# Kernel tuning notes

Measured on AMD Instinct MI355X. Metric: run time of the kernel, lower is better.

The kernel has to match this reference:

```python
import jax, jax.numpy as jnp
import numpy as np

C = 256; NH = 8; HD = C // NH; NL = 4; NP = 4; DFF = 1024
B = 8; NQ = 900
SHAPES = ((100, 100), (50, 50), (25, 25), (13, 13))
LEN = sum(h * w for h, w in SHAPES)


def setup_inputs() -> dict:
    key = jax.random.key(0)
    ks = jax.random.split(key, 16)
    s = 0.02
    d = {}
    d['tgt'] = jax.random.normal(ks[0], (B, NQ, C), jnp.float32)
    d['query_pos'] = jax.random.normal(ks[1], (B, NQ, C), jnp.float32)
    d['reference_points'] = jax.random.uniform(ks[2], (B, NQ, NL, 2), jnp.float32)
    d['src'] = jax.random.normal(ks[3], (B, LEN, C), jnp.float32)
    d['spatial_shapes'] = np.array(SHAPES, dtype=np.int32)
    # self-attn (nn.MultiheadAttention) params, stored [in,out]
    d['sa_in_w'] = jax.random.normal(ks[4], (C, 3 * C), jnp.float32) * s
    d['sa_in_b'] = jnp.zeros((3 * C,), jnp.float32)
    d['sa_out_w'] = jax.random.normal(ks[5], (C, C), jnp.float32) * s
    d['sa_out_b'] = jnp.zeros((C,), jnp.float32)
    d['ln2_g'] = jnp.ones((C,), jnp.float32); d['ln2_b'] = jnp.zeros((C,), jnp.float32)
    # MSDeformAttn params
    d['off_w'] = jax.random.normal(ks[6], (C, NH * NL * NP * 2), jnp.float32) * s
    d['off_b'] = jax.random.normal(ks[7], (NH * NL * NP * 2,), jnp.float32) * 0.5
    d['attw_w'] = jax.random.normal(ks[8], (C, NH * NL * NP), jnp.float32) * s
    d['attw_b'] = jnp.zeros((NH * NL * NP,), jnp.float32)
    d['val_w'] = jax.random.normal(ks[9], (C, C), jnp.float32) * s
    d['val_b'] = jnp.zeros((C,), jnp.float32)
    d['proj_w'] = jax.random.normal(ks[10], (C, C), jnp.float32) * s
    d['proj_b'] = jnp.zeros((C,), jnp.float32)
    d['ln1_g'] = jnp.ones((C,), jnp.float32); d['ln1_b'] = jnp.zeros((C,), jnp.float32)
    # FFN
    d['lin1_w'] = jax.random.normal(ks[11], (C, DFF), jnp.float32) * s
    d['lin1_b'] = jnp.zeros((DFF,), jnp.float32)
    d['lin2_w'] = jax.random.normal(ks[12], (DFF, C), jnp.float32) * s
    d['lin2_b'] = jnp.zeros((C,), jnp.float32)
    d['ln3_g'] = jnp.ones((C,), jnp.float32); d['ln3_b'] = jnp.zeros((C,), jnp.float32)
    return d


def _ln(x, g, b):
    m = jnp.mean(x, -1, keepdims=True)
    v = jnp.mean((x - m) ** 2, -1, keepdims=True)
    return (x - m) * jax.lax.rsqrt(v + 1e-5) * g + b


def _bilinear(v, loc, H, W):
    # v: [B,NH,H*W,HD]; loc: [B,NQ,NH,NP,2] normalized to [0,1]
    # matches F.grid_sample(align_corners=False, padding_mode='zeros')
    b = v.shape[0]; nq = loc.shape[1]
    x = loc[..., 0] * W - 0.5
    y = loc[..., 1] * H - 0.5
    x0 = jnp.floor(x); y0 = jnp.floor(y)
    dx = x - x0; dy = y - y0
    x0i = x0.astype(jnp.int32); y0i = y0.astype(jnp.int32)

    def gat(ix, iy):
        valid = ((ix >= 0) & (ix < W) & (iy >= 0) & (iy < H)).astype(v.dtype)
        idx = jnp.clip(iy, 0, H - 1) * W + jnp.clip(ix, 0, W - 1)  # [B,NQ,NH,NP]
        idx_t = jnp.transpose(idx, (0, 2, 1, 3)).reshape(b, NH, nq * NP)
        g = jnp.take_along_axis(v, idx_t[..., None], axis=2).reshape(b, NH, nq, NP, HD)
        return g * jnp.transpose(valid, (0, 2, 1, 3))[..., None]

    wt = lambda a: jnp.transpose(a, (0, 2, 1, 3))[..., None]
    return (gat(x0i, y0i) * wt((1 - dx) * (1 - dy))
            + gat(x0i + 1, y0i) * wt(dx * (1 - dy))
            + gat(x0i, y0i + 1) * wt((1 - dx) * dy)
            + gat(x0i + 1, y0i + 1) * wt(dx * dy))


def _msda(q, ref, src, shapes, val_w, val_b, off_w, off_b, attw_w, attw_b, proj_w, proj_b):
    b, nq, _ = q.shape
    value = jnp.transpose((src @ val_w + val_b).reshape(b, -1, NH, HD), (0, 2, 1, 3))  # [B,NH,Len,HD]
    off = (q @ off_w + off_b).reshape(b, nq, NH, NL, NP, 2)
    aw = jax.nn.softmax((q @ attw_w + attw_b).reshape(b, nq, NH, NL * NP), -1)
    aw = aw.reshape(b, nq, NH, NL, NP)
    acc = jnp.zeros((b, NH, nq, HD), q.dtype)
    start = 0
    for l, (H_, W_) in enumerate(shapes):
        norm = jnp.array([W_, H_], q.dtype)
        loc = ref[:, :, None, l, None, :] + off[:, :, :, l] / norm  # [B,NQ,NH,NP,2]
        smp = _bilinear(value[:, :, start:start + H_ * W_], loc, H_, W_)  # [B,NH,NQ,NP,HD]
        acc = acc + jnp.sum(smp * jnp.transpose(aw[:, :, :, l], (0, 2, 1, 3))[..., None], axis=3)
        start += H_ * W_
    out = jnp.transpose(acc, (0, 2, 1, 3)).reshape(b, nq, C)
    return out @ proj_w + proj_b


def _self_attn(x, pos, in_w, in_b, out_w, out_b):
    b, nq, _ = x.shape
    qk = x + pos
    q = (qk @ in_w[:, :C] + in_b[:C]).reshape(b, nq, NH, HD)
    k = (qk @ in_w[:, C:2 * C] + in_b[C:2 * C]).reshape(b, nq, NH, HD)
    v = (x @ in_w[:, 2 * C:] + in_b[2 * C:]).reshape(b, nq, NH, HD)
    att = jax.nn.softmax(jnp.einsum('bqhd,bkhd->bhqk', q, k) * (1.0 / float(np.sqrt(HD))), -1)
    o = jnp.einsum('bhqk,bkhd->bqhd', att, v).reshape(b, nq, C)
    return o @ out_w + out_b


def _forward(tgt, query_pos, reference_points, src, shapes,
             sa_in_w, sa_in_b, sa_out_w, sa_out_b, ln2_g, ln2_b,
             off_w, off_b, attw_w, attw_b, val_w, val_b, proj_w, proj_b, ln1_g, ln1_b,
             lin1_w, lin1_b, lin2_w, lin2_b, ln3_g, ln3_b):
    t2 = _self_attn(tgt, query_pos, sa_in_w, sa_in_b, sa_out_w, sa_out_b)
    t = _ln(tgt + t2, ln2_g, ln2_b)
    t2 = _msda(t + query_pos, reference_points, src, shapes,
               val_w, val_b, off_w, off_b, attw_w, attw_b, proj_w, proj_b)
    t = _ln(t + t2, ln1_g, ln1_b)
    h = jax.nn.relu(t @ lin1_w + lin1_b) @ lin2_w + lin2_b
    return _ln(t + h, ln3_g, ln3_b)


def reference(tgt, query_pos, reference_points, src, spatial_shapes,
              sa_in_w, sa_in_b, sa_out_w, sa_out_b, ln2_g, ln2_b,
              off_w, off_b, attw_w, attw_b, val_w, val_b, proj_w, proj_b, ln1_g, ln1_b,
              lin1_w, lin1_b, lin2_w, lin2_b, ln3_g, ln3_b):
    shapes = [(int(h), int(w)) for h, w in np.asarray(spatial_shapes)]
    return _forward(tgt, query_pos, reference_points, src, shapes,
                    sa_in_w, sa_in_b, sa_out_w, sa_out_b, ln2_g, ln2_b,
                    off_w, off_b, attw_w, attw_b, val_w, val_b, proj_w, proj_b, ln1_g, ln1_b,
                    lin1_w, lin1_b, lin2_w, lin2_b, ln3_g, ln3_b)
```

## Files before the change

### kernel.cpp

```cpp
#include <hip/hip_runtime.h>
#include <hip/hip_bf16.h>
#include <type_traits>

#define C_DIM 256
#define NHEAD 8
#define HDIM 32
#define NLVL 4
#define NPT 4
#define DFF_DIM 1024
#define BB 8
#define NQ_DIM 900
#define LEN_DIM 13294
#define ROWS (BB * NQ_DIM)
#define VROWS (BB * LEN_DIM)
#define VT_LD 928

typedef __attribute__((ext_vector_type(8))) short short8v;
typedef __attribute__((ext_vector_type(8))) unsigned short ushort8v;
typedef __attribute__((ext_vector_type(4))) float float4v;
typedef __attribute__((ext_vector_type(4))) unsigned short ushort4v;

__device__ __forceinline__ float bf2f(unsigned short u) {
  union { unsigned int i; float f; } v; v.i = ((unsigned int)u) << 16; return v.f;
}
__device__ __forceinline__ unsigned short f2bf(float f) {
  __hip_bfloat16 h = __float2bfloat16(f);
  return *reinterpret_cast<unsigned short*>(&h);
}

#define WCONV_BLOCKS 2048
__global__ __launch_bounds__(256) void wprep_kernel(
    const float* __restrict__ w0, const float* __restrict__ w1,
    const float* __restrict__ w2, const float* __restrict__ w3,
    const float* __restrict__ w4, const float* __restrict__ w5,
    const float* __restrict__ w6, const float* __restrict__ w7,
    unsigned short* __restrict__ out,
    const float* __restrict__ tgt, const float* __restrict__ qpos,
    unsigned short* __restrict__ tgtbf, unsigned short* __restrict__ x0bf, int n4) {
  int bid = blockIdx.x;
  if (bid < WCONV_BLOCKS) {
    const int Ks[8] = {256, 256, 256, 256, 256, 256, 256, 1024};
    const int Ns[8] = {768, 256, 256, 128, 256, 256, 1024, 256};
    const int Oo[8] = {0, 196608, 262144, 327680, 360448, 425984, 491520, 753664};
    int w = bid >> 8, bx = bid & 255;
    int K = Ks[w], N = Ns[w];
    int ntx = N >> 5, nty = K >> 5;
    if (bx >= ntx * nty) return;
    int tx = bx % ntx, ty = bx / ntx;
    const float* W = w == 0 ? w0 : w == 1 ? w1 : w == 2 ? w2 : w == 3 ? w3
                   : w == 4 ? w4 : w == 5 ? w5 : w == 6 ? w6 : w7;
    __shared__ float tile[32][33];
    int c = threadIdx.x & 31, rg = threadIdx.x >> 5;
#pragma unroll
    for (int j = 0; j < 4; ++j) {
      int k = ty * 32 + rg * 4 + j;
      tile[rg * 4 + j][c] = W[(size_t)k * N + tx * 32 + c];
    }
    __syncthreads();
    unsigned short* o = out + Oo[w];
#pragma unroll
    for (int j = 0; j < 4; ++j) {
      int n = tx * 32 + rg * 4 + j;
      o[(size_t)n * K + ty * 32 + c] = f2bf(tile[c][rg * 4 + j]);
    }
  } else {
    int i = (bid - WCONV_BLOCKS) * 256 + threadIdx.x;
    if (i < n4) {
      float4 x = reinterpret_cast<const float4*>(tgt)[i];
      float4 y = reinterpret_cast<const float4*>(qpos)[i];
      ushort4v u1, u2;
      u1[0] = f2bf(x.x); u1[1] = f2bf(x.y); u1[2] = f2bf(x.z); u1[3] = f2bf(x.w);
      u2[0] = f2bf(x.x + y.x); u2[1] = f2bf(x.y + y.y);
      u2[2] = f2bf(x.z + y.z); u2[3] = f2bf(x.w + y.w);
      *reinterpret_cast<ushort4v*>(tgtbf + (size_t)i * 4) = u1;
      *reinterpret_cast<ushort4v*>(x0bf + (size_t)i * 4) = u2;
    }
  }
}

template <typename TA, typename TO, int RELU>
__device__ __forceinline__ void gemm_body(
    unsigned short* smem,
    const TA* __restrict__ A, const TA* __restrict__ A2,
    const unsigned short* __restrict__ Wt,
    const float* __restrict__ bias, const float* __restrict__ bias2,
    TO* __restrict__ Cout, TO* __restrict__ Cout2,
    int M, int N, int K, int lda, int ldc, int ldc2, int colSplit,
    int bx, int by) {
  auto Al = reinterpret_cast<unsigned short(*)[128][40]>(smem);
  auto Wl = reinterpret_cast<unsigned short(*)[128][40]>(smem + 10240);
  const int tid = threadIdx.x;
  const int lane = tid & 63, wid = tid >> 6;
  const int g = lane >> 4, ql = lane & 15;
  const int wr = wid >> 1, wc = wid & 1;
  const int row0 = by * 128, col0 = bx * 128;

  const TA* Ause = (A2 != nullptr && col0 >= colSplit) ? A2 : A;

  float4v acc[4][4];
#pragma unroll
  for (int i = 0; i < 4; ++i)
#pragma unroll
    for (int j = 0; j < 4; ++j) acc[i][j] = (float4v){0.f, 0.f, 0.f, 0.f};

  float4 areg_f[4];
  ushort8v areg_b[2];
  ushort8v wreg[2];

  auto loadA = [&](int k0) {
    if constexpr (std::is_same<TA, float>::value) {
#pragma unroll
      for (int j = 0; j < 4; ++j) {
        int c = tid + 256 * j;
        int row = c >> 3, f4 = c & 7;
        int gr = min(row0 + row, M - 1);
        areg_f[j] = *reinterpret_cast<const float4*>(Ause + (size_t)gr * lda + k0 + f4 * 4);
      }
    } else {
#pragma unroll
      for (int j = 0; j < 2; ++j) {
        int c = tid + 256 * j;
        int row = c >> 2, ch = c & 3;
        int gr = min(row0 + row, M - 1);
        areg_b[j] = *reinterpret_cast<const ushort8v*>(
            reinterpret_cast<const unsigned short*>(Ause) + (size_t)gr * lda + k0 + ch * 8);
      }
    }
  };
  auto loadW = [&](int k0) {
#pragma unroll
    for (int j = 0; j < 2; ++j) {
      int c = tid + 256 * j;
      int row = c >> 2, ch = c & 3;
      wreg[j] = *reinterpret_cast<const ushort8v*>(
          Wt + (size_t)(col0 + row) * K + k0 + ch * 8);
    }
  };
  auto storeA = [&](int buf) {
    if constexpr (std::is_same<TA, float>::value) {
#pragma unroll
      for (int j = 0; j < 4; ++j) {
        int c = tid + 256 * j;
        int row = c >> 3, f4 = c & 7;
        ushort4v u;
        u[0] = f2bf(areg_f[j].x); u[1] = f2bf(areg_f[j].y);
        u[2] = f2bf(areg_f[j].z); u[3] = f2bf(areg_f[j].w);
        *reinterpret_cast<ushort4v*>(&Al[buf][row][f4 * 4]) = u;
      }
    } else {
#pragma unroll
      for (int j = 0; j < 2; ++j) {
        int c = tid + 256 * j;
        int row = c >> 2, ch = c & 3;
        *reinterpret_cast<ushort8v*>(&Al[buf][row][ch * 8]) = areg_b[j];
      }
    }
  };
  auto storeW = [&](int buf) {
#pragma unroll
    for (int j = 0; j < 2; ++j) {
      int c = tid + 256 * j;
      int row = c >> 2, ch = c & 3;
      *reinterpret_cast<ushort8v*>(&Wl[buf][row][ch * 8]) = wreg[j];
    }
  };

  const int nt = K >> 5;
  loadA(0); loadW(0);
  storeA(0); storeW(0);

  for (int t = 0; t < nt; ++t) {
    __syncthreads();
    if (t + 1 < nt) { loadA((t + 1) << 5); loadW((t + 1) << 5); }
    const int cur = t & 1;
    short8v af[4], bfr[4];
#pragma unroll
    for (int mi = 0; mi < 4; ++mi)
      af[mi] = *reinterpret_cast<const short8v*>(&Al[cur][wr * 64 + mi * 16 + ql][8 * g]);
#pragma unroll
    for (int ni = 0; ni < 4; ++ni)
      bfr[ni] = *reinterpret_cast<const short8v*>(&Wl[cur][wc * 64 + ni * 16 + ql][8 * g]);
#pragma unroll
    for (int mi = 0; mi < 4; ++mi)
#pragma unroll
      for (int ni = 0; ni < 4; ++ni)
        acc[mi][ni] = __builtin_amdgcn_mfma_f32_16x16x32_bf16(af[mi], bfr[ni], acc[mi][ni], 0, 0, 0);
    if (t + 1 < nt) { storeA(cur ^ 1); storeW(cur ^ 1); }
  }

  const bool sel2 = (Cout2 != nullptr && col0 >= colSplit);
  const float* bsrc = sel2 ? bias2 : bias;
  TO* outp = sel2 ? Cout2 : Cout;
  const int ldco = sel2 ? ldc2 : ldc;
  const int cbase = sel2 ? (col0 - colSplit) : col0;
  float bv[4];
#pragma unroll
  for (int ni = 0; ni < 4; ++ni) bv[ni] = bsrc[cbase + wc * 64 + ni * 16 + ql];
#pragma unroll
  for (int mi = 0; mi < 4; ++mi) {
#pragma unroll
    for (int r = 0; r < 4; ++r) {
      int row = row0 + wr * 64 + mi * 16 + 4 * g + r;
      if (row >= M) continue;
#pragma unroll
      for (int ni = 0; ni < 4; ++ni) {
        int col = cbase + wc * 64 + ni * 16 + ql;
        float v = acc[mi][ni][r] + bv[ni];
        if (RELU) v = fmaxf(v, 0.f);
        if constexpr (std::is_same<TO, float>::value) {
          outp[(size_t)row * ldco + col] = v;
        } else {
          outp[(size_t)row * ldco + col] = __float2bfloat16(v);
        }
      }
    }
  }
}

template <typename TA, typename TO, int RELU>
__global__ __launch_bounds__(256) void mfma_gemm_kernel(
    const TA* __restrict__ A, const TA* __restrict__ A2,
    const unsigned short* __restrict__ Wt,
    const float* __restrict__ bias, const float* __restrict__ bias2,
    TO* __restrict__ Cout, TO* __restrict__ Cout2,
    int M, int N, int K, int lda, int ldc, int ldc2, int colSplit) {
  __shared__ unsigned short smem[20480];
  gemm_body<TA, TO, RELU>(smem, A, A2, Wt, bias, bias2, Cout, Cout2,
                          M, N, K, lda, ldc, ldc2, colSplit,
                          blockIdx.x, blockIdx.y);
}

#define QKV_BLOCKS (6 * 57)
__global__ __launch_bounds__(256) void qkv_value_kernel(
    const unsigned short* __restrict__ x0bf, const unsigned short* __restrict__ tgtbf,
    const unsigned short* __restrict__ sa_inT, const float* __restrict__ sa_in_b,
    __hip_bfloat16* __restrict__ qkbuf, __hip_bfloat16* __restrict__ vbuf,
    const float* __restrict__ src, const unsigned short* __restrict__ valT,
    const float* __restrict__ val_b, __hip_bfloat16* __restrict__ value) {
  __shared__ unsigned short smem[20480];
  int bid = blockIdx.x;
  if (bid < QKV_BLOCKS) {
    gemm_body<unsigned short, __hip_bfloat16, 0>(
        smem, x0bf, tgtbf, sa_inT, sa_in_b, sa_in_b + 512, qkbuf, vbuf,
        ROWS, 768, 256, 256, 512, 256, 512, bid % 6, bid / 6);
  } else {
    int t = bid - QKV_BLOCKS;
    gemm_body<float, __hip_bfloat16, 0>(
        smem, src, nullptr, valT, val_b, nullptr, value, nullptr,
        VROWS, 256, 256, 256, 256, 0, 1 << 30, t & 1, t >> 1);
  }
}

__global__ __launch_bounds__(256) void vtrans_kernel(
    const unsigned short* __restrict__ vbuf, unsigned short* __restrict__ vT) {
  __shared__ unsigned short tile[32][34];
  int b = blockIdx.y;
  int ct = blockIdx.x & 7;
  int rt = blockIdx.x >> 3;
  int rl = threadIdx.x >> 3, c4 = (threadIdx.x & 7) * 4;
  int gr = min(rt * 32 + rl, NQ_DIM - 1);
  ushort4v v = *reinterpret_cast<const ushort4v*>(
      vbuf + ((size_t)(b * NQ_DIM + gr)) * 256 + ct * 32 + c4);
  tile[rl][c4] = v[0]; tile[rl][c4 + 1] = v[1];
  tile[rl][c4 + 2] = v[2]; tile[rl][c4 + 3] = v[3];
  __syncthreads();
  int cl = threadIdx.x >> 3, r4 = (threadIdx.x & 7) * 4;
  ushort4v o;
  o[0] = tile[r4][cl]; o[1] = tile[r4 + 1][cl];
  o[2] = tile[r4 + 2][cl]; o[3] = tile[r4 + 3][cl];
  *reinterpret_cast<ushort4v*>(
      vT + ((size_t)b * 256 + ct * 32 + cl) * VT_LD + rt * 32 + r4) = o;
}

__global__ __launch_bounds__(256) void ln_fused_kernel(const float* __restrict__ x,
                                                       const float* __restrict__ y,
                                                       const float* __restrict__ gg,
                                                       const float* __restrict__ bb,
                                                       float* __restrict__ out,
                                                       unsigned short* __restrict__ out2,
                                                       const float* __restrict__ qadd) {
  int row = blockIdx.x, t = threadIdx.x;
  size_t base = (size_t)row * C_DIM + t;
  float v = x[base] + y[base];
  float s = v, s2 = v * v;
#pragma unroll
  for (int o = 32; o > 0; o >>= 1) {
    s += __shfl_xor(s, o);
    s2 += __shfl_xor(s2, o);
  }
  __shared__ float w1[4], w2[4];
  int wid = t >> 6, lane = t & 63;
  if (lane == 0) { w1[wid] = s; w2[wid] = s2; }
  __syncthreads();
  float S = w1[0] + w1[1] + w1[2] + w1[3];
  float S2 = w2[0] + w2[1] + w2[2] + w2[3];
  float mean = S * (1.f / 256.f);
  float var = S2 * (1.f / 256.f) - mean * mean;
  float rstd = rsqrtf(var + 1e-5f);
  float r = (v - mean) * rstd * gg[t] + bb[t];
  out[base] = r;
  if (out2) {
    float r2 = qadd ? (r + qadd[base]) : r;
    out2[base] = f2bf(r2);
  }
}

__global__ __launch_bounds__(256) void self_attn_mfma_kernel(
    const unsigned short* __restrict__ qk, const unsigned short* __restrict__ vT,
    unsigned short* __restrict__ out) {
  __shared__ unsigned short P_lds[4][16][32];
  const int tid = threadIdx.x;
  const int lane = tid & 63, wid = tid >> 6;
  const int g = lane >> 4, ql = lane & 15;
  const int bh = blockIdx.y;
  const int b = bh >> 3, h = bh & 7;
  const int q0 = blockIdx.x * 64 + wid * 16;
  const float scale = 0.17677669529663687f;

  const unsigned short* qk_b = qk + (size_t)b * NQ_DIM * 512;
  const int qrow = min(q0 + ql, NQ_DIM - 1);
  short8v qf = *reinterpret_cast<const short8v*>(
      qk_b + (size_t)qrow * 512 + h * HDIM + 8 * g);
  const unsigned short* kb = qk_b + 256 + h * HDIM + 8 * g;
  const unsigned short* vtb0 = vT + ((size_t)b * 256 + h * HDIM + ql) * VT_LD;
  const unsigned short* vtb1 = vtb0 + 16 * VT_LD;

  float4v o0 = {0.f, 0.f, 0.f, 0.f}, o1 = {0.f, 0.f, 0.f, 0.f};
  float m = -1e30f, lsum = 0.f;

  const int NT = 29;
  for (int kt = 0; kt < NT; ++kt) {
    const int k_base = kt * 32;
    int kr0 = min(k_base + ql, NQ_DIM - 1);
    int kr1 = min(k_base + 16 + ql, NQ_DIM - 1);
    short8v kf0 = *reinterpret_cast<const short8v*>(kb + (size_t)kr0 * 512);
    short8v kf1 = *reinterpret_cast<const short8v*>(kb + (size_t)kr1 * 512);
    float4v z = {0.f, 0.f, 0.f, 0.f};
    float4v s0 = __builtin_amdgcn_mfma_f32_16x16x32_bf16(kf0, qf, z, 0, 0, 0);
    float4v s1 = __builtin_amdgcn_mfma_f32_16x16x32_bf16(kf1, qf, z, 0, 0, 0);

    float s[8];
#pragma unroll
    for (int r = 0; r < 4; ++r) { s[r] = s0[r] * scale; s[4 + r] = s1[r] * scale; }
    if (kt == NT - 1) {
#pragma unroll
      for (int i = 0; i < 8; ++i) {
        int kk = k_base + 16 * (i >> 2) + 4 * g + (i & 3);
        if (kk >= NQ_DIM) s[i] = -1e30f;
      }
    }
    float tm = s[0];
#pragma unroll
    for (int i = 1; i < 8; ++i) tm = fmaxf(tm, s[i]);
    tm = fmaxf(tm, __shfl_xor(tm, 16));
    tm = fmaxf(tm, __shfl_xor(tm, 32));
    float mnew = fmaxf(m, tm);
    float alpha = __expf(m - mnew);
    float p[8];
    float ts = 0.f;
#pragma unroll
    for (int i = 0; i < 8; ++i) { p[i] = __expf(s[i] - mnew); ts += p[i]; }
    ts += __shfl_xor(ts, 16);
    ts += __shfl_xor(ts, 32);
    lsum = lsum * alpha + ts;
    m = mnew;

    ushort4v pp0, pp1;
#pragma unroll
    for (int r = 0; r < 4; ++r) { pp0[r] = f2bf(p[r]); pp1[r] = f2bf(p[4 + r]); }
    *reinterpret_cast<ushort4v*>(&P_lds[wid][ql][4 * g]) = pp0;
    *reinterpret_cast<ushort4v*>(&P_lds[wid][ql][16 + 4 * g]) = pp1;
    asm volatile("s_waitcnt lgkmcnt(0)" ::: "memory");
    __builtin_amdgcn_sched_barrier(0);

    o0 *= alpha;
    o1 *= alpha;

    short8v pf = *reinterpret_cast<const short8v*>(&P_lds[wid][ql][8 * g]);
    short8v vf0 = *reinterpret_cast<const short8v*>(vtb0 + k_base + 8 * g);
    short8v vf1 = *reinterpret_cast<const short8v*>(vtb1 + k_base + 8 * g);
    o0 = __builtin_amdgcn_mfma_f32_16x16x32_bf16(vf0, pf, o0, 0, 0, 0);
    o1 = __builtin_amdgcn_mfma_f32_16x16x32_bf16(vf1, pf, o1, 0, 0, 0);
  }

  float inv = 1.f / lsum;
  if (q0 + ql < NQ_DIM) {
    unsigned short* op = out + ((size_t)(b * NQ_DIM) + q0 + ql) * C_DIM + h * HDIM;
    ushort4v u0, u1;
#pragma unroll
    for (int r = 0; r < 4; ++r) { u0[r] = f2bf(o0[r] * inv); u1[r] = f2bf(o1[r] * inv); }
    *reinterpret_cast<ushort4v*>(op + 4 * g) = u0;
    *reinterpret_cast<ushort4v*>(op + 16 + 4 * g) = u1;
  }
}

__global__ __launch_bounds__(256) void softmax16_kernel(float* __restrict__ aw, int total) {
  int t = blockIdx.x * 256 + threadIdx.x;
  if (t >= total) return;
  float* p = aw + (size_t)t * 16;
  float vals[16];
  float m = -1e30f;
#pragma unroll
  for (int i = 0; i < 16; ++i) { vals[i] = p[i]; m = fmaxf(m, vals[i]); }
  float s = 0.f;
#pragma unroll
  for (int i = 0; i < 16; ++i) { vals[i] = __expf(vals[i] - m); s += vals[i]; }
  float inv = 1.f / s;
#pragma unroll
  for (int i = 0; i < 16; ++i) p[i] = vals[i] * inv;
}

__global__ __launch_bounds__(256) void msda_sample_kernel(
    const unsigned short* __restrict__ value,
    const float* __restrict__ off,
    const float* __restrict__ aw,
    const float* __restrict__ refp,
    const int* __restrict__ shapes,
    unsigned short* __restrict__ out) {
  int g = blockIdx.x * 64 + (threadIdx.x >> 2);
  int d8 = threadIdx.x & 3;
  int h = g & 7;
  int row = g >> 3;
  int b = row / NQ_DIM;
  float acc[8] = {};
  int start = 0;
  const float* offr = off + (size_t)row * 256 + h * 32;
  const float* awr  = aw + (size_t)row * 128 + h * 16;
  const float* rpr  = refp + (size_t)row * NLVL * 2;
#pragma unroll
  for (int l = 0; l < NLVL; ++l) {
    int Hl = shapes[2 * l], Wl = shapes[2 * l + 1];
    float fx = rpr[2 * l + 0] * (float)Wl - 0.5f;
    float fy = rpr[2 * l + 1] * (float)Hl - 0.5f;
    const unsigned short* vbase =
        value + ((size_t)(b * LEN_DIM + start)) * C_DIM + h * HDIM + d8 * 8;
#pragma unroll
    for (int p = 0; p < NPT; ++p) {
      float x = fx + offr[l * 8 + p * 2];
      float y = fy + offr[l * 8 + p * 2 + 1];
      float a = awr[l * 4 + p];
      float x0f = floorf(x), y0f = floorf(y);
      float dx = x - x0f, dy = y - y0f;
      int x0 = (int)x0f, y0 = (int)y0f;
      int x1 = x0 + 1, y1 = y0 + 1;
      float wx1 = dx, wx0 = 1.f - dx;
      float wy1 = dy * a, wy0 = (1.f - dy) * a;
      bool vx0 = ((unsigned)x0 < (unsigned)Wl);
      bool vx1 = ((unsigned)x1 < (unsigned)Wl);
      bool vy0 = ((unsigned)y0 < (unsigned)Hl);
      bool vy1 = ((unsigned)y1 < (unsigned)Hl);
      float w00 = (vx0 && vy0) ? wx0 * wy0 : 0.f;
      float w10 = (vx1 && vy0) ? wx1 * wy0 : 0.f;
      float w01 = (vx0 && vy1) ? wx0 * wy1 : 0.f;
      float w11 = (vx1 && vy1) ? wx1 * wy1 : 0.f;
      int x0c = min(max(x0, 0), Wl - 1), x1c = min(max(x1, 0), Wl - 1);
      int y0c = min(max(y0, 0), Hl - 1), y1c = min(max(y1, 0), Hl - 1);
      int r0 = y0c * Wl, r1 = y1c * Wl;
      ushort8v g00 = *reinterpret_cast<const ushort8v*>(vbase + ((r0 + x0c) << 8));
      ushort8v g10 = *reinterpret_cast<const ushort8v*>(vbase + ((r0 + x1c) << 8));
      ushort8v g01 = *reinterpret_cast<const ushort8v*>(vbase + ((r1 + x0c) << 8));
      ushort8v g11 = *reinterpret_cast<const ushort8v*>(vbase + ((r1 + x1c) << 8));
#pragma unroll
      for (int j = 0; j < 8; ++j)
        acc[j] += w00 * bf2f(g00[j]) + w10 * bf2f(g10[j]) +
                  w01 * bf2f(g01[j]) + w11 * bf2f(g11[j]);
    }
    start += Hl * Wl;
  }
  ushort8v o;
#pragma unroll
  for (int j = 0; j < 8; ++j) o[j] = f2bf(acc[j]);
  *reinterpret_cast<ushort8v*>(out + (size_t)row * C_DIM + h * HDIM + d8 * 8) = o;
}

extern "C" void kernel_launch(void* const* d_in, const int* in_sizes, int n_in,
                              void* d_out, int out_size, void* d_ws, size_t ws_size,
                              hipStream_t stream) {
  const float* tgt      = (const float*)d_in[0];
  const float* qpos     = (const float*)d_in[1];
  const float* refp     = (const float*)d_in[2];
  const float* src      = (const float*)d_in[3];
  const int*   shapes   = (const int*)d_in[4];
  const float* sa_in_w  = (const float*)d_in[5];
  const float* sa_in_b  = (const float*)d_in[6];
  const float* sa_out_w = (const float*)d_in[7];
  const float* sa_out_b = (const float*)d_in[8];
  const float* ln2_g    = (const float*)d_in[9];
  const float* ln2_b    = (const float*)d_in[10];
  const float* off_w    = (const float*)d_in[11];
  const float* off_b    = (const float*)d_in[12];
  const float* attw_w   = (const float*)d_in[13];
  const float* attw_b   = (const float*)d_in[14];
  const float* val_w    = (const float*)d_in[15];
  const float* val_b    = (const float*)d_in[16];
  const float* proj_w   = (const float*)d_in[17];
  const float* proj_b   = (const float*)d_in[18];
  const float* ln1_g    = (const float*)d_in[19];
  const float* ln1_b    = (const float*)d_in[20];
  const float* lin1_w   = (const float*)d_in[21];
  const float* lin1_b   = (const float*)d_in[22];
  const float* lin2_w   = (const float*)d_in[23];
  const float* lin2_b   = (const float*)d_in[24];
  const float* ln3_g    = (const float*)d_in[25];
  const float* ln3_b    = (const float*)d_in[26];

  char* ws = (char*)d_ws;
  size_t off_b_ws = 0;
  auto alloc = [&](size_t bytes) {
    char* p = ws + off_b_ws;
    off_b_ws += (bytes + 255) & ~(size_t)255;
    return p;
  };
  unsigned short* wT     = (unsigned short*)alloc((size_t)1015808 * 2);
  unsigned short* value  = (unsigned short*)alloc((size_t)VROWS * C_DIM * 2);
  unsigned short* qkbuf  = (unsigned short*)alloc((size_t)ROWS * 512 * 2);
  unsigned short* vbuf   = (unsigned short*)alloc((size_t)ROWS * 256 * 2);
  unsigned short* vTbuf  = (unsigned short*)alloc((size_t)BB * 256 * VT_LD * 2);
  unsigned short* tgtbf  = (unsigned short*)alloc((size_t)ROWS * C_DIM * 2);
  unsigned short* X0bf   = (unsigned short*)alloc((size_t)ROWS * C_DIM * 2);
  unsigned short* attnbf = (unsigned short*)alloc((size_t)ROWS * C_DIM * 2);
  unsigned short* X3bf   = (unsigned short*)alloc((size_t)ROWS * C_DIM * 2);
  unsigned short* sampbf = (unsigned short*)alloc((size_t)ROWS * C_DIM * 2);
  unsigned short* X6bf   = (unsigned short*)alloc((size_t)ROWS * C_DIM * 2);
  unsigned short* hidbf  = (unsigned short*)alloc((size_t)ROWS * DFF_DIM * 2);
  float* X1 = (float*)alloc((size_t)ROWS * C_DIM * 4);
  float* X2 = (float*)alloc((size_t)ROWS * C_DIM * 4);
  float* X4 = (float*)alloc((size_t)ROWS * C_DIM * 4);
  float* X5 = (float*)alloc((size_t)ROWS * 128 * 4);
  float* X6 = (float*)alloc((size_t)ROWS * C_DIM * 4);
  if (off_b_ws > ws_size) return;

  unsigned short* sa_inT = wT + 0;
  unsigned short* sa_outT = wT + 196608;
  unsigned short* offT   = wT + 262144;
  unsigned short* valT   = wT + 360448;
  unsigned short* projT  = wT + 425984;
  unsigned short* lin1T  = wT + 491520;
  unsigned short* lin2T  = wT + 753664;

  dim3 blk(256);
  const int MB7200 = (ROWS + 127) / 128;
  const int MBV = (VROWS + 127) / 128;
  int n4 = ROWS * C_DIM / 4;
  int prepBlocks = (n4 + 255) / 256;

  wprep_kernel<<<WCONV_BLOCKS + prepBlocks, blk, 0, stream>>>(
      sa_in_w, sa_out_w, off_w, attw_w, val_w, proj_w, lin1_w, lin2_w, wT,
      tgt, qpos, tgtbf, X0bf, n4);

  qkv_value_kernel<<<QKV_BLOCKS + 2 * MBV, blk, 0, stream>>>(
      X0bf, tgtbf, sa_inT, sa_in_b, (__hip_bfloat16*)qkbuf, (__hip_bfloat16*)vbuf,
      src, valT, val_b, (__hip_bfloat16*)value);

  vtrans_kernel<<<dim3(8 * 29, BB), blk, 0, stream>>>(vbuf, vTbuf);

  self_attn_mfma_kernel<<<dim3(15, 64), blk, 0, stream>>>(qkbuf, vTbuf, attnbf);
  mfma_gemm_kernel<unsigned short, float, 0><<<dim3(2, MB7200), blk, 0, stream>>>(
      attnbf, nullptr, sa_outT, sa_out_b, nullptr,
      X1, nullptr, ROWS, 256, 256, 256, 256, 0, 1 << 30);
  ln_fused_kernel<<<ROWS, blk, 0, stream>>>(tgt, X1, ln2_g, ln2_b, X2, X3bf, qpos);

  mfma_gemm_kernel<unsigned short, float, 0><<<dim3(3, MB7200), blk, 0, stream>>>(
      X3bf, nullptr, offT, off_b, attw_b,
      X4, X5, ROWS, 384, 256, 256, 256, 128, 256);
  softmax16_kernel<<<(ROWS * NHEAD + 255) / 256, blk, 0, stream>>>(X5, ROWS * NHEAD);
  msda_sample_kernel<<<ROWS * NHEAD / 64, blk, 0, stream>>>(
      value, X4, X5, refp, shapes, sampbf);
  mfma_gemm_kernel<unsigned short, float, 0><<<dim3(2, MB7200), blk, 0, stream>>>(
      sampbf, nullptr, projT, proj_b, nullptr,
      X1, nullptr, ROWS, 256, 256, 256, 256, 0, 1 << 30);
  ln_fused_kernel<<<ROWS, blk, 0, stream>>>(X2, X1, ln1_g, ln1_b, X6, X6bf, nullptr);

  mfma_gemm_kernel<unsigned short, __hip_bfloat16, 1><<<dim3(8, MB7200), blk, 0, stream>>>(
      X6bf, nullptr, lin1T, lin1_b, nullptr,
      (__hip_bfloat16*)hidbf, nullptr, ROWS, 1024, 256, 256, 1024, 0, 1 << 30);
  mfma_gemm_kernel<unsigned short, float, 0><<<dim3(2, MB7200), blk, 0, stream>>>(
      hidbf, nullptr, lin2T, lin2_b, nullptr,
      X1, nullptr, ROWS, 256, 1024, 1024, 256, 0, 1 << 30);
  ln_fused_kernel<<<ROWS, blk, 0, stream>>>(X6, X1, ln3_g, ln3_b, (float*)d_out, nullptr, nullptr);
}
```

Before: 225.6 us.

## Use 64x64 GEMM tiles for small GEMMs and co-schedule value projection with self-attention

Adds a 64x64-tile GEMM variant and uses it for the QKV, output-projection, offset, proj and FFN GEMMs, which gives 4x more blocks for the 7200-row matrices to fill the CUs. The value-projection GEMM moves out of the QKV launch and into a combined launch with the self-attention blocks, so the large independent value GEMM overlaps with attention. The smaller tiles trade more grid parallelism for less data reuse per block and more redundant global loads.

Result: slower. 231.6 us (+2.7%).

```diff
diff --git a/kernel.cpp b/kernel.cpp
--- a/kernel.cpp
+++ b/kernel.cpp
@@ -81,11 +81,11 @@
 template <typename TA, typename TO, int RELU>
 __device__ __forceinline__ void gemm_body(
     unsigned short* smem,
-    const TA* __restrict__ A, const TA* __restrict__ A2,
+    const TA* __restrict__ A,
     const unsigned short* __restrict__ Wt,
-    const float* __restrict__ bias, const float* __restrict__ bias2,
-    TO* __restrict__ Cout, TO* __restrict__ Cout2,
-    int M, int N, int K, int lda, int ldc, int ldc2, int colSplit,
+    const float* __restrict__ bias,
+    TO* __restrict__ Cout,
+    int M, int N, int K, int lda, int ldc,
     int bx, int by) {
   auto Al = reinterpret_cast<unsigned short(*)[128][40]>(smem);
   auto Wl = reinterpret_cast<unsigned short(*)[128][40]>(smem + 10240);
@@ -95,8 +95,6 @@
   const int wr = wid >> 1, wc = wid & 1;
   const int row0 = by * 128, col0 = bx * 128;
 
-  const TA* Ause = (A2 != nullptr && col0 >= colSplit) ? A2 : A;
-
   float4v acc[4][4];
 #pragma unroll
   for (int i = 0; i < 4; ++i)
@@ -114,7 +112,7 @@
         int c = tid + 256 * j;
         int row = c >> 3, f4 = c & 7;
         int gr = min(row0 + row, M - 1);
-        areg_f[j] = *reinterpret_cast<const float4*>(Ause + (size_t)gr * lda + k0 + f4 * 4);
+        areg_f[j] = *reinterpret_cast<const float4*>(A + (size_t)gr * lda + k0 + f4 * 4);
       }
     } else {
 #pragma unroll
@@ -123,7 +121,7 @@
         int row = c >> 2, ch = c & 3;
         int gr = min(row0 + row, M - 1);
         areg_b[j] = *reinterpret_cast<const ushort8v*>(
-            reinterpret_cast<const unsigned short*>(Ause) + (size_t)gr * lda + k0 + ch * 8);
+            reinterpret_cast<const unsigned short*>(A) + (size_t)gr * lda + k0 + ch * 8);
       }
     }
   };
@@ -188,23 +186,139 @@
     if (t + 1 < nt) { storeA(cur ^ 1); storeW(cur ^ 1); }
   }
 
+  float bv[4];
+#pragma unroll
+  for (int ni = 0; ni < 4; ++ni) bv[ni] = bias[col0 + wc * 64 + ni * 16 + ql];
+#pragma unroll
+  for (int mi = 0; mi < 4; ++mi) {
+#pragma unroll
+    for (int r = 0; r < 4; ++r) {
+      int row = row0 + wr * 64 + mi * 16 + 4 * g + r;
+      if (row >= M) continue;
+#pragma unroll
+      for (int ni = 0; ni < 4; ++ni) {
+        int col = col0 + wc * 64 + ni * 16 + ql;
+        float v = acc[mi][ni][r] + bv[ni];
+        if (RELU) v = fmaxf(v, 0.f);
+        if constexpr (std::is_same<TO, float>::value) {
+          Cout[(size_t)row * ldc + col] = v;
+        } else {
+          Cout[(size_t)row * ldc + col] = __float2bfloat16(v);
+        }
+      }
+    }
+  }
+}
+
+template <typename TA, typename TO, int RELU>
+__device__ __forceinline__ void gemm_body64(
+    unsigned short* smem,
+    const TA* __restrict__ A, const TA* __restrict__ A2,
+    const unsigned short* __restrict__ Wt,
+    const float* __restrict__ bias, const float* __restrict__ bias2,
+    TO* __restrict__ Cout, TO* __restrict__ Cout2,
+    int M, int N, int K, int lda, int ldc, int ldc2, int colSplit,
+    int bx, int by) {
+  auto Al = reinterpret_cast<unsigned short(*)[64][40]>(smem);
+  auto Wl = reinterpret_cast<unsigned short(*)[64][40]>(smem + 5120);
+  const int tid = threadIdx.x;
+  const int lane = tid & 63, wid = tid >> 6;
+  const int g = lane >> 4, ql = lane & 15;
+  const int wr = wid >> 1, wc = wid & 1;
+  const int row0 = by * 64, col0 = bx * 64;
+
+  const TA* Ause = (A2 != nullptr && col0 >= colSplit) ? A2 : A;
+
+  float4v acc[2][2];
+#pragma unroll
+  for (int i = 0; i < 2; ++i)
+#pragma unroll
+    for (int j = 0; j < 2; ++j) acc[i][j] = (float4v){0.f, 0.f, 0.f, 0.f};
+
+  float4 areg_f[2];
+  ushort8v areg_b;
+  ushort8v wreg;
+  const int a_row = tid >> 2, a_ch = tid & 3;
+  const int f_row = tid >> 3, f_f4 = tid & 7;
+
+  auto loadA = [&](int k0) {
+    if constexpr (std::is_same<TA, float>::value) {
+#pragma unroll
+      for (int j = 0; j < 2; ++j) {
+        int c = tid + 256 * j;
+        int row = c >> 3, f4 = c & 7;
+        int gr = min(row0 + row, M - 1);
+        areg_f[j] = *reinterpret_cast<const float4*>(Ause + (size_t)gr * lda + k0 + f4 * 4);
+      }
+    } else {
+      int gr = min(row0 + a_row, M - 1);
+      areg_b = *reinterpret_cast<const ushort8v*>(
+          reinterpret_cast<const unsigned short*>(Ause) + (size_t)gr * lda + k0 + a_ch * 8);
+    }
+  };
+  auto loadW = [&](int k0) {
+    wreg = *reinterpret_cast<const ushort8v*>(
+        Wt + (size_t)(col0 + a_row) * K + k0 + a_ch * 8);
+  };
+  auto storeA = [&](int buf) {
+    if constexpr (std::is_same<TA, float>::value) {
+#pragma unroll
+      for (int j = 0; j < 2; ++j) {
+        int c = tid + 256 * j;
+        int row = c >> 3, f4 = c & 7;
+        ushort4v u;
+        u[0] = f2bf(areg_f[j].x); u[1] = f2bf(areg_f[j].y);
+        u[2] = f2bf(areg_f[j].z); u[3] = f2bf(areg_f[j].w);
+        *reinterpret_cast<ushort4v*>(&Al[buf][row][f4 * 4]) = u;
+      }
+    } else {
+      *reinterpret_cast<ushort8v*>(&Al[buf][a_row][a_ch * 8]) = areg_b;
+    }
+  };
+  auto storeW = [&](int buf) {
+    *reinterpret_cast<ushort8v*>(&Wl[buf][a_row][a_ch * 8]) = wreg;
+  };
+
+  const int nt = K >> 5;
+  loadA(0); loadW(0);
+  storeA(0); storeW(0);
+
+  for (int t = 0; t < nt; ++t) {
+    __syncthreads();
+    if (t + 1 < nt) { loadA((t + 1) << 5); loadW((t + 1) << 5); }
+    const int cur = t & 1;
+    short8v af[2], bfr[2];
+#pragma unroll
+    for (int mi = 0; mi < 2; ++mi)
+      af[mi] = *reinterpret_cast<const short8v*>(&Al[cur][wr * 32 + mi * 16 + ql][8 * g]);
+#pragma unroll
+    for (int ni = 0; ni < 2; ++ni)
+      bfr[ni] = *reinterpret_cast<const short8v*>(&Wl[cur][wc * 32 + ni * 16 + ql][8 * g]);
+#pragma unroll
+    for (int mi = 0; mi < 2; ++mi)
+#pragma unroll
+      for (int ni = 0; ni < 2; ++ni)
+        acc[mi][ni] = __builtin_amdgcn_mfma_f32_16x16x32_bf16(af[mi], bfr[ni], acc[mi][ni], 0, 0, 0);
+    if (t + 1 < nt) { storeA(cur ^ 1); storeW(cur ^ 1); }
+  }
+
   const bool sel2 = (Cout2 != nullptr && col0 >= colSplit);
   const float* bsrc = sel2 ? bias2 : bias;
   TO* outp = sel2 ? Cout2 : Cout;
   const int ldco = sel2 ? ldc2 : ldc;
   const int cbase = sel2 ? (col0 - colSplit) : col0;
-  float bv[4];
-#pragma unroll
-  for (int ni = 0; ni < 4; ++ni) bv[ni] = bsrc[cbase + wc * 64 + ni * 16 + ql];
-#pragma unroll
-  for (int mi = 0; mi < 4; ++mi) {
+  float bv[2];
+#pragma unroll
+  for (int ni = 0; ni < 2; ++ni) bv[ni] = bsrc[cbase + wc * 32 + ni * 16 + ql];
+#pragma unroll
+  for (int mi = 0; mi < 2; ++mi) {
 #pragma unroll
     for (int r = 0; r < 4; ++r) {
-      int row = row0 + wr * 64 + mi * 16 + 4 * g + r;
+      int row = row0 + wr * 32 + mi * 16 + 4 * g + r;
       if (row >= M) continue;
 #pragma unroll
-      for (int ni = 0; ni < 4; ++ni) {
-        int col = cbase + wc * 64 + ni * 16 + ql;
+      for (int ni = 0; ni < 2; ++ni) {
+        int col = cbase + wc * 32 + ni * 16 + ql;
         float v = acc[mi][ni][r] + bv[ni];
         if (RELU) v = fmaxf(v, 0.f);
         if constexpr (std::is_same<TO, float>::value) {
@@ -218,36 +332,122 @@
 }
 
 template <typename TA, typename TO, int RELU>
-__global__ __launch_bounds__(256) void mfma_gemm_kernel(
+__global__ __launch_bounds__(256) void mfma_gemm64_kernel(
     const TA* __restrict__ A, const TA* __restrict__ A2,
     const unsigned short* __restrict__ Wt,
     const float* __restrict__ bias, const float* __restrict__ bias2,
     TO* __restrict__ Cout, TO* __restrict__ Cout2,
     int M, int N, int K, int lda, int ldc, int ldc2, int colSplit) {
-  __shared__ unsigned short smem[20480];
-  gemm_body<TA, TO, RELU>(smem, A, A2, Wt, bias, bias2, Cout, Cout2,
-                          M, N, K, lda, ldc, ldc2, colSplit,
-                          blockIdx.x, blockIdx.y);
-}
-
-#define QKV_BLOCKS (6 * 57)
-__global__ __launch_bounds__(256) void qkv_value_kernel(
-    const unsigned short* __restrict__ x0bf, const unsigned short* __restrict__ tgtbf,
-    const unsigned short* __restrict__ sa_inT, const float* __restrict__ sa_in_b,
-    __hip_bfloat16* __restrict__ qkbuf, __hip_bfloat16* __restrict__ vbuf,
+  __shared__ unsigned short smem[10240];
+  gemm_body64<TA, TO, RELU>(smem, A, A2, Wt, bias, bias2, Cout, Cout2,
+                            M, N, K, lda, ldc, ldc2, colSplit,
+                            blockIdx.x, blockIdx.y);
+}
+
+__device__ __forceinline__ void attn_body(
+    unsigned short* smem,
+    const unsigned short* __restrict__ qk, const unsigned short* __restrict__ vT,
+    unsigned short* __restrict__ out, int qt, int bh) {
+  auto P_lds = reinterpret_cast<unsigned short(*)[16][32]>(smem);
+  const int tid = threadIdx.x;
+  const int lane = tid & 63, wid = tid >> 6;
+  const int g = lane >> 4, ql = lane & 15;
+  const int b = bh >> 3, h = bh & 7;
+  const int q0 = qt * 64 + wid * 16;
+  const float scale = 0.17677669529663687f;
+
+  const unsigned short* qk_b = qk + (size_t)b * NQ_DIM * 512;
+  const int qrow = min(q0 + ql, NQ_DIM - 1);
+  short8v qf = *reinterpret_cast<const short8v*>(
+      qk_b + (size_t)qrow * 512 + h * HDIM + 8 * g);
+  const unsigned short* kb = qk_b + 256 + h * HDIM + 8 * g;
+  const unsigned short* vtb0 = vT + ((size_t)b * 256 + h * HDIM + ql) * VT_LD;
+  const unsigned short* vtb1 = vtb0 + 16 * VT_LD;
+
+  float4v o0 = {0.f, 0.f, 0.f, 0.f}, o1 = {0.f, 0.f, 0.f, 0.f};
+  float m = -1e30f, lsum = 0.f;
+
+  const int NT = 29;
+  for (int kt = 0; kt < NT; ++kt) {
+    const int k_base = kt * 32;
+    int kr0 = min(k_base + ql, NQ_DIM - 1);
+    int kr1 = min(k_base + 16 + ql, NQ_DIM - 1);
+    short8v kf0 = *reinterpret_cast<const short8v*>(kb + (size_t)kr0 * 512);
+    short8v kf1 = *reinterpret_cast<const short8v*>(kb + (size_t)kr1 * 512);
+    float4v z = {0.f, 0.f, 0.f, 0.f};
+    float4v s0 = __builtin_amdgcn_mfma_f32_16x16x32_bf16(kf0, qf, z, 0, 0, 0);
+    float4v s1 = __builtin_amdgcn_mfma_f32_16x16x32_bf16(kf1, qf, z, 0, 0, 0);
+
+    float s[8];
+#pragma unroll
+    for (int r = 0; r < 4; ++r) { s[r] = s0[r] * scale; s[4 + r] = s1[r] * scale; }
+    if (kt == NT - 1) {
+#pragma unroll
+      for (int i = 0; i < 8; ++i) {
+        int kk = k_base + 16 * (i >> 2) + 4 * g + (i & 3);
+        if (kk >= NQ_DIM) s[i] = -1e30f;
+      }
+    }
+    float tm = s[0];
+#pragma unroll
+    for (int i = 1; i < 8; ++i) tm = fmaxf(tm, s[i]);
+    tm = fmaxf(tm, __shfl_xor(tm, 16));
+    tm = fmaxf(tm, __shfl_xor(tm, 32));
+    float mnew = fmaxf(m, tm);
+    float alpha = __expf(m - mnew);
+    float p[8];
+    float ts = 0.f;
+#pragma unroll
+    for (int i = 0; i < 8; ++i) { p[i] = __expf(s[i] - mnew); ts += p[i]; }
+    ts += __shfl_xor(ts, 16);
+    ts += __shfl_xor(ts, 32);
+    lsum = lsum * alpha + ts;
+    m = mnew;
+
+    ushort4v pp0, pp1;
+#pragma unroll
+    for (int r = 0; r < 4; ++r) { pp0[r] = f2bf(p[r]); pp1[r] = f2bf(p[4 + r]); }
+    *reinterpret_cast<ushort4v*>(&P_lds[wid][ql][4 * g]) = pp0;
+    *reinterpret_cast<ushort4v*>(&P_lds[wid][ql][16 + 4 * g]) = pp1;
+    asm volatile("s_waitcnt lgkmcnt(0)" ::: "memory");
+    __builtin_amdgcn_sched_barrier(0);
+
+    o0 *= alpha;
+    o1 *= alpha;
+
+    short8v pf = *reinterpret_cast<const short8v*>(&P_lds[wid][ql][8 * g]);
+    short8v vf0 = *reinterpret_cast<const short8v*>(vtb0 + k_base + 8 * g);
+    short8v vf1 = *reinterpret_cast<const short8v*>(vtb1 + k_base + 8 * g);
+    o0 = __builtin_amdgcn_mfma_f32_16x16x32_bf16(vf0, pf, o0, 0, 0, 0);
+    o1 = __builtin_amdgcn_mfma_f32_16x16x32_bf16(vf1, pf, o1, 0, 0, 0);
+  }
+
+  float inv = 1.f / lsum;
+  if (q0 + ql < NQ_DIM) {
+    unsigned short* op = out + ((size_t)(b * NQ_DIM) + q0 + ql) * C_DIM + h * HDIM;
+    ushort4v u0, u1;
+#pragma unroll
+    for (int r = 0; r < 4; ++r) { u0[r] = f2bf(o0[r] * inv); u1[r] = f2bf(o1[r] * inv); }
+    *reinterpret_cast<ushort4v*>(op + 4 * g) = u0;
+    *reinterpret_cast<ushort4v*>(op + 16 + 4 * g) = u1;
+  }
+}
+
+#define VAL_BLOCKS (2 * 831)
+__global__ __launch_bounds__(256) void value_attn_kernel(
     const float* __restrict__ src, const unsigned short* __restrict__ valT,
-    const float* __restrict__ val_b, __hip_bfloat16* __restrict__ value) {
+    const float* __restrict__ val_b, __hip_bfloat16* __restrict__ value,
+    const unsigned short* __restrict__ qkbuf, const unsigned short* __restrict__ vTbuf,
+    unsigned short* __restrict__ attnout) {
   __shared__ unsigned short smem[20480];
   int bid = blockIdx.x;
-  if (bid < QKV_BLOCKS) {
-    gemm_body<unsigned short, __hip_bfloat16, 0>(
-        smem, x0bf, tgtbf, sa_inT, sa_in_b, sa_in_b + 512, qkbuf, vbuf,
-        ROWS, 768, 256, 256, 512, 256, 512, bid % 6, bid / 6);
+  if (bid < VAL_BLOCKS) {
+    gemm_body<float, __hip_bfloat16, 0>(
+        smem, src, valT, val_b, value,
+        VROWS, 256, 256, 256, 256, bid & 1, bid >> 1);
   } else {
-    int t = bid - QKV_BLOCKS;
-    gemm_body<float, __hip_bfloat16, 0>(
-        smem, src, nullptr, valT, val_b, nullptr, value, nullptr,
-        VROWS, 256, 256, 256, 256, 0, 1 << 30, t & 1, t >> 1);
+    int a = bid - VAL_BLOCKS;
+    attn_body(smem, qkbuf, vTbuf, attnout, a % 15, a / 15);
   }
 }
 
@@ -302,95 +502,6 @@
   if (out2) {
     float r2 = qadd ? (r + qadd[base]) : r;
     out2[base] = f2bf(r2);
-  }
-}
-
-__global__ __launch_bounds__(256) void self_attn_mfma_kernel(
-    const unsigned short* __restrict__ qk, const unsigned short* __restrict__ vT,
-    unsigned short* __restrict__ out) {
-  __shared__ unsigned short P_lds[4][16][32];
-  const int tid = threadIdx.x;
-  const int lane = tid & 63, wid = tid >> 6;
-  const int g = lane >> 4, ql = lane & 15;
-  const int bh = blockIdx.y;
-  const int b = bh >> 3, h = bh & 7;
-  const int q0 = blockIdx.x * 64 + wid * 16;
-  const float scale = 0.17677669529663687f;
-
-  const unsigned short* qk_b = qk + (size_t)b * NQ_DIM * 512;
-  const int qrow = min(q0 + ql, NQ_DIM - 1);
-  short8v qf = *reinterpret_cast<const short8v*>(
-      qk_b + (size_t)qrow * 512 + h * HDIM + 8 * g);
-  const unsigned short* kb = qk_b + 256 + h * HDIM + 8 * g;
-  const unsigned short* vtb0 = vT + ((size_t)b * 256 + h * HDIM + ql) * VT_LD;
-  const unsigned short* vtb1 = vtb0 + 16 * VT_LD;
-
-  float4v o0 = {0.f, 0.f, 0.f, 0.f}, o1 = {0.f, 0.f, 0.f, 0.f};
-  float m = -1e30f, lsum = 0.f;
-
-  const int NT = 29;
-  for (int kt = 0; kt < NT; ++kt) {
-    const int k_base = kt * 32;
-    int kr0 = min(k_base + ql, NQ_DIM - 1);
-    int kr1 = min(k_base + 16 + ql, NQ_DIM - 1);
-    short8v kf0 = *reinterpret_cast<const short8v*>(kb + (size_t)kr0 * 512);
-    short8v kf1 = *reinterpret_cast<const short8v*>(kb + (size_t)kr1 * 512);
-    float4v z = {0.f, 0.f, 0.f, 0.f};
-    float4v s0 = __builtin_amdgcn_mfma_f32_16x16x32_bf16(kf0, qf, z, 0, 0, 0);
-    float4v s1 = __builtin_amdgcn_mfma_f32_16x16x32_bf16(kf1, qf, z, 0, 0, 0);
-
-    float s[8];
-#pragma unroll
-    for (int r = 0; r < 4; ++r) { s[r] = s0[r] * scale; s[4 + r] = s1[r] * scale; }
-    if (kt == NT - 1) {
-#pragma unroll
-      for (int i = 0; i < 8; ++i) {
-        int kk = k_base + 16 * (i >> 2) + 4 * g + (i & 3);
-        if (kk >= NQ_DIM) s[i] = -1e30f;
-      }
-    }
-    float tm = s[0];
-#pragma unroll
-    for (int i = 1; i < 8; ++i) tm = fmaxf(tm, s[i]);
-    tm = fmaxf(tm, __shfl_xor(tm, 16));
-    tm = fmaxf(tm, __shfl_xor(tm, 32));
-    float mnew = fmaxf(m, tm);
-    float alpha = __expf(m - mnew);
-    float p[8];
-    float ts = 0.f;
-#pragma unroll
-    for (int i = 0; i < 8; ++i) { p[i] = __expf(s[i] - mnew); ts += p[i]; }
-    ts += __shfl_xor(ts, 16);
-    ts += __shfl_xor(ts, 32);
-    lsum = lsum * alpha + ts;
-    m = mnew;
-
-    ushort4v pp0, pp1;
-#pragma unroll
-    for (int r = 0; r < 4; ++r) { pp0[r] = f2bf(p[r]); pp1[r] = f2bf(p[4 + r]); }
-    *reinterpret_cast<ushort4v*>(&P_lds[wid][ql][4 * g]) = pp0;
-    *reinterpret_cast<ushort4v*>(&P_lds[wid][ql][16 + 4 * g]) = pp1;
-    asm volatile("s_waitcnt lgkmcnt(0)" ::: "memory");
-    __builtin_amdgcn_sched_barrier(0);
-
-    o0 *= alpha;
-    o1 *= alpha;
-
-    short8v pf = *reinterpret_cast<const short8v*>(&P_lds[wid][ql][8 * g]);
-    short8v vf0 = *reinterpret_cast<const short8v*>(vtb0 + k_base + 8 * g);
-    short8v vf1 = *reinterpret_cast<const short8v*>(vtb1 + k_base + 8 * g);
-    o0 = __builtin_amdgcn_mfma_f32_16x16x32_bf16(vf0, pf, o0, 0, 0, 0);
-    o1 = __builtin_amdgcn_mfma_f32_16x16x32_bf16(vf1, pf, o1, 0, 0, 0);
-  }
-
-  float inv = 1.f / lsum;
-  if (q0 + ql < NQ_DIM) {
-    unsigned short* op = out + ((size_t)(b * NQ_DIM) + q0 + ql) * C_DIM + h * HDIM;
-    ushort4v u0, u1;
-#pragma unroll
-    for (int r = 0; r < 4; ++r) { u0[r] = f2bf(o0[r] * inv); u1[r] = f2bf(o1[r] * inv); }
-    *reinterpret_cast<ushort4v*>(op + 4 * g) = u0;
-    *reinterpret_cast<ushort4v*>(op + 16 + 4 * g) = u1;
   }
 }
 
@@ -539,8 +650,7 @@
   unsigned short* lin2T  = wT + 753664;
 
   dim3 blk(256);
-  const int MB7200 = (ROWS + 127) / 128;
-  const int MBV = (VROWS + 127) / 128;
+  const int MB64 = (ROWS + 63) / 64;
   int n4 = ROWS * C_DIM / 4;
   int prepBlocks = (n4 + 255) / 256;
 
@@ -548,33 +658,35 @@
       sa_in_w, sa_out_w, off_w, attw_w, val_w, proj_w, lin1_w, lin2_w, wT,
       tgt, qpos, tgtbf, X0bf, n4);
 
-  qkv_value_kernel<<<QKV_BLOCKS + 2 * MBV, blk, 0, stream>>>(
-      X0bf, tgtbf, sa_inT, sa_in_b, (__hip_bfloat16*)qkbuf, (__hip_bfloat16*)vbuf,
-      src, valT, val_b, (__hip_bfloat16*)value);
+  mfma_gemm64_kernel<unsigned short, __hip_bfloat16, 0><<<dim3(12, MB64), blk, 0, stream>>>(
+      X0bf, tgtbf, sa_inT, sa_in_b, sa_in_b + 512,
+      (__hip_bfloat16*)qkbuf, (__hip_bfloat16*)vbuf, ROWS, 768, 256, 256, 512, 256, 512);
 
   vtrans_kernel<<<dim3(8 * 29, BB), blk, 0, stream>>>(vbuf, vTbuf);
 
-  self_attn_mfma_kernel<<<dim3(15, 64), blk, 0, stream>>>(qkbuf, vTbuf, attnbf);
-  mfma_gemm_kernel<unsigned short, float, 0><<<dim3(2, MB7200), blk, 0, stream>>>(
+  value_attn_kernel<<<VAL_BLOCKS + 15 * 64, blk, 0, stream>>>(
+      src, valT, val_b, (__hip_bfloat16*)value, qkbuf, vTbuf, attnbf);
+
+  mfma_gemm64_kernel<unsigned short, float, 0><<<dim3(4, MB64), blk, 0, stream>>>(
       attnbf, nullptr, sa_outT, sa_out_b, nullptr,
       X1, nullptr, ROWS, 256, 256, 256, 256, 0, 1 << 30);
   ln_fused_kernel<<<ROWS, blk, 0, stream>>>(tgt, X1, ln2_g, ln2_b, X2, X3bf, qpos);
 
-  mfma_gemm_kernel<unsigned short, float, 0><<<dim3(3, MB7200), blk, 0, stream>>>(
+  mfma_gemm64_kernel<unsigned short, float, 0><<<dim3(6, MB64), blk, 0, stream>>>(
       X3bf, nullptr, offT, off_b, attw_b,
       X4, X5, ROWS, 384, 256, 256, 256, 128, 256);
   softmax16_kernel<<<(ROWS * NHEAD + 255) / 256, blk, 0, stream>>>(X5, ROWS * NHEAD);
   msda_sample_kernel<<<ROWS * NHEAD / 64, blk, 0, stream>>>(
       value, X4, X5, refp, shapes, sampbf);
-  mfma_gemm_kernel<unsigned short, float, 0><<<dim3(2, MB7200), blk, 0, stream>>>(
+  mfma_gemm64_kernel<unsigned short, float, 0><<<dim3(4, MB64), blk, 0, stream>>>(
       sampbf, nullptr, projT, proj_b, nullptr,
       X1, nullptr, ROWS, 256, 256, 256, 256, 0, 1 << 30);
   ln_fused_kernel<<<ROWS, blk, 0, stream>>>(X2, X1, ln1_g, ln1_b, X6, X6bf, nullptr);
 
-  mfma_gemm_kernel<unsigned short, __hip_bfloat16, 1><<<dim3(8, MB7200), blk, 0, stream>>>(
+  mfma_gemm64_kernel<unsigned short, __hip_bfloat16, 1><<<dim3(16, MB64), blk, 0, stream>>>(
       X6bf, nullptr, lin1T, lin1_b, nullptr,
       (__hip_bfloat16*)hidbf, nullptr, ROWS, 1024, 256, 256, 1024, 0, 1 << 30);
-  mfma_gemm_kernel<unsigned short, float, 0><<<dim3(2, MB7200), blk, 0, stream>>>(
+  mfma_gemm64_kernel<unsigned short, float, 0><<<dim3(4, MB64), blk, 0, stream>>>(
       hidbf, nullptr, lin2T, lin2_b, nullptr,
       X1, nullptr, ROWS, 256, 1024, 1024, 256, 0, 1 << 30);
   ln_fused_kernel<<<ROWS, blk, 0, stream>>>(X6, X1, ln3_g, ln3_b, (float*)d_out, nullptr, nullptr);
```
